# Kernel tuning notes

Measured on AMD Instinct MI355X. Metric: run time of the kernel, lower is better.

Reference implementation:

```python
import jax, jax.numpy as jnp
import numpy as np

N, DIN, HID, DOUT = 8192, 256, 256, 128   # nodes, gcn dims
B, L = 64, 64                              # ragged batch, max seq len
LH, C = 128, 4                             # lstm hidden, n_classes


def setup_inputs() -> dict:
    key = jax.random.key(0)
    ks = jax.random.split(key, 12)
    s = lambda k, shape, fan: jax.random.normal(k, shape, jnp.float32) / np.float32(np.sqrt(fan))
    A = jax.random.normal(ks[0], (N, N), jnp.float32) / np.float32(np.sqrt(N))
    X = jax.random.normal(ks[1], (N, DIN), jnp.float32)
    token_ids = jax.random.randint(ks[2], (B, L), 0, N, dtype=jnp.int32)
    lengths = jax.random.randint(ks[3], (B,), 1, L + 1, dtype=jnp.int32)
    return {
        'A': A, 'X': X, 'token_ids': token_ids, 'lengths': lengths,
        'W1': s(ks[4], (DIN, HID), DIN), 'b1': jnp.zeros((HID,), jnp.float32),
        'W2': s(ks[5], (HID, DOUT), HID), 'b2': jnp.zeros((DOUT,), jnp.float32),
        'Wih_f': s(ks[6], (4 * LH, DOUT), DOUT), 'Whh_f': s(ks[7], (4 * LH, LH), LH),
        'b_f': jnp.zeros((4 * LH,), jnp.float32),
        'Wih_b': s(ks[8], (4 * LH, DOUT), DOUT), 'Whh_b': s(ks[9], (4 * LH, LH), LH),
        'b_b': jnp.zeros((4 * LH,), jnp.float32),
        'Wfc': s(ks[10], (C, 2 * LH), 2 * LH), 'bfc': jnp.zeros((C,), jnp.float32),
    }


def _lstm_final(xp, mask, Whh):
    """xp: [L,B,4H] precomputed input gates, mask: [L,B]. Returns final valid h [B,H]."""
    Bsz = xp.shape[1]
    h0 = jnp.zeros((Bsz, Whh.shape[1]), xp.dtype)

    def step(carry, inp):
        h, c = carry
        xg, m = inp
        gates = xg + h @ Whh.T
        i, f, g, o = jnp.split(gates, 4, axis=-1)   # torch gate order i,f,g,o
        c_new = jax.nn.sigmoid(f) * c + jax.nn.sigmoid(i) * jnp.tanh(g)
        h_new = jax.nn.sigmoid(o) * jnp.tanh(c_new)
        m = m[:, None]
        return (jnp.where(m, h_new, h), jnp.where(m, c_new, c)), None

    (h, _), _ = jax.lax.scan(step, (h0, h0), (xp, mask))
    return h


def reference(A, X, token_ids, lengths, W1, b1, W2, b2,
              Wih_f, Whh_f, b_f, Wih_b, Whh_b, b_b, Wfc, bfc):
    # 2-layer GCN (num_layer=2 -> no middle layers / no relu); dropout in eval mode
    H1 = A @ (X @ W1) + b1                 # [N, HID]
    Hn = A @ (H1 @ W2) + b2                # [N, DOUT]
    seqs = Hn[token_ids]                   # ragged gather -> [B, L, DOUT]
    mask = (jnp.arange(L)[None, :] < lengths[:, None]).T            # [L, B]
    xp_f = jnp.einsum('bld,gd->lbg', seqs, Wih_f) + b_f             # [L, B, 4H]
    xp_b = jnp.einsum('bld,gd->lbg', seqs[:, ::-1], Wih_b) + b_b
    # backward dir: reversing a right-padded seq puts padding first; mask keeps
    # state frozen until the valid region, so final h == backward-final hidden.
    h_f = _lstm_final(xp_f, mask, Whh_f)
    h_b = _lstm_final(xp_b, mask[::-1], Whh_b)
    return jnp.concatenate([h_f, h_b], axis=-1) @ Wfc.T + bfc       # [B, C]
```

## Files before the change

kernel.cpp:

```cpp
#include <hip/hip_runtime.h>
#include <hip/hip_bf16.h>


typedef float f32x4 __attribute__((ext_vector_type(4)));
typedef __bf16 bf16x8 __attribute__((ext_vector_type(8)));
typedef unsigned short u16;
typedef unsigned int u32;

__device__ __forceinline__ u16 bf_hi_rn(float x, float& rem) {
    u32 u = __builtin_bit_cast(u32, x);
    u32 r = u + 0x7FFFu + ((u >> 16) & 1u);
    u16 h = (u16)(r >> 16);
    float hf = __builtin_bit_cast(float, (u32)h << 16);
    rem = x - hf;
    return h;
}
__device__ __forceinline__ u16 bf_trunc(float x) {
    return (u16)(__builtin_bit_cast(u32, x) >> 16);
}
__device__ __forceinline__ void pack8(const float* v, uint4& H, uint4& L) {
    u32 h[4], l[4];
#pragma unroll
    for (int q = 0; q < 4; q++) {
        float r0, r1;
        u32 h0 = bf_hi_rn(v[2 * q], r0);
        u32 h1 = bf_hi_rn(v[2 * q + 1], r1);
        h[q] = h0 | (h1 << 16);
        l[q] = (u32)bf_trunc(r0) | ((u32)bf_trunc(r1) << 16);
    }
    H = make_uint4(h[0], h[1], h[2], h[3]);
    L = make_uint4(l[0], l[1], l[2], l[3]);
}

__device__ __forceinline__ void glds16(const u16* g, u16* l) {
    __builtin_amdgcn_global_load_lds(
        (const __attribute__((address_space(1))) void*)g,
        (__attribute__((address_space(3))) void*)l, 16, 0, 0);
}

template<int TRANS>
__global__ void wsplit_k(const float* __restrict__ W, u16* __restrict__ hi,
                         u16* __restrict__ lo, int K, int N) {
    int gid = blockIdx.x * 256 + threadIdx.x;
    int total = (K >> 5) * N * 4;
    if (gid >= total) return;
    int g = gid & 3, n = (gid >> 2) % N, kc = gid / (4 * N);
    float v[8];
#pragma unroll
    for (int e = 0; e < 8; e++) {
        int k = kc * 32 + g * 8 + e;
        v[e] = TRANS ? W[(size_t)k * N + n] : W[(size_t)n * K + k];
    }
    uint4 H, L;
    pack8(v, H, L);
    int p = g ^ ((n >> 1) & 3);
    size_t off = ((size_t)kc * N + n) * 32 + p * 8;
    *(uint4*)(hi + off) = H;
    *(uint4*)(lo + off) = L;
}

template<int GMODE, int NPART, int BIASA, int SPLITOUT, int BIASC, int DUAL>
__global__ __launch_bounds__(512, 1) void gemm2_k(
    const float* __restrict__ A, int ldA, int Mtot,
    const u16* __restrict__ Bhi, const u16* __restrict__ Blo,
    const u16* __restrict__ Bhi2, const u16* __restrict__ Blo2, int Nfull,
    float* __restrict__ C, int ldC, long partStride,
    u16* __restrict__ Chi, u16* __restrict__ Clo, int Nout,
    const float* __restrict__ biasA,
    const float* __restrict__ biasC, const float* __restrict__ biasC2,
    const int* __restrict__ tok, int kchunk, int Mhalf)
{
    constexpr int BM = 256, BN = 128;
    const int t = threadIdx.x;
    const int lane = t & 63, wv = t >> 6;
    const int fm = lane & 15, fq = lane >> 4;
    const int wm0 = (wv >> 1) * 64, wn0 = (wv & 1) * 64;
    const int m0 = blockIdx.x * BM;
    const int n0 = blockIdx.z * BN;
    const int kbeg = blockIdx.y * kchunk;

    __shared__ alignas(16) u16 sAhi[2][BM * 32];
    __shared__ alignas(16) u16 sAlo[2][BM * 32];
    __shared__ alignas(16) u16 sBhi[2][BN * 32];
    __shared__ alignas(16) u16 sBlo[2][BN * 32];
    __shared__ int sRow[BM];

    if (t < BM) {
        int r;
        if (GMODE == 0) r = m0 + t;
        else if (GMODE == 1) r = tok[m0 + t];
        else {
            int trip = m0 + t;
            int rem = trip & (Mhalf - 1);
            int l = rem >> 6, b = rem & 63;
            r = (trip < Mhalf) ? (b * 64 + l) : (b * 64 + (63 - l));
        }
        sRow[t] = r;
    }
    __syncthreads();

    const bool second = DUAL && (m0 >= Mhalf);
    const u16* __restrict__ bhp = second ? Bhi2 : Bhi;
    const u16* __restrict__ blp = second ? Blo2 : Blo;

    const int r = t >> 1, half = t & 1, co = half * 16;
    const int sw = (r >> 1) & 3;
    const int p0 = (2 * half) ^ sw, p1 = (2 * half + 1) ^ sw;
    const float* Abase = A + (size_t)sRow[r] * ldA + co;
    const size_t pstep = (size_t)Mtot * ldA;

    const size_t bstep = (size_t)Nfull * 32;
    const u16* gbh = bhp + ((size_t)(kbeg >> 5) * Nfull + n0) * 32 + t * 8;
    const u16* gbl = blp + ((size_t)(kbeg >> 5) * Nfull + n0) * 32 + t * 8;
    u16* ldsBh0 = &sBhi[0][wv * 512];
    u16* ldsBl0 = &sBlo[0][wv * 512];
    u16* ldsBh1 = &sBhi[1][wv * 512];
    u16* ldsBl1 = &sBlo[1][wv * 512];

    f32x4 acc[4][4];
#pragma unroll
    for (int i = 0; i < 4; i++)
#pragma unroll
        for (int j = 0; j < 4; j++) acc[i][j] = (f32x4){0.f, 0.f, 0.f, 0.f};

    float av[16];
    auto loadA = [&](int kk) {
#pragma unroll
        for (int c = 0; c < 16; c += 4) {
            float4 s = *(const float4*)(Abase + kk + c);
            av[c] = s.x; av[c + 1] = s.y; av[c + 2] = s.z; av[c + 3] = s.w;
        }
#pragma unroll
        for (int p = 1; p < NPART; p++) {
#pragma unroll
            for (int c = 0; c < 16; c += 4) {
                float4 s = *(const float4*)(Abase + (size_t)p * pstep + kk + c);
                av[c] += s.x; av[c + 1] += s.y; av[c + 2] += s.z; av[c + 3] += s.w;
            }
        }
        if (BIASA) {
#pragma unroll
            for (int c = 0; c < 16; c += 4) {
                float4 s = *(const float4*)(biasA + kk + co + c);
                av[c] += s.x; av[c + 1] += s.y; av[c + 2] += s.z; av[c + 3] += s.w;
            }
        }
    };
    auto storeA = [&](int nb) {
        uint4 H0, L0, H1, L1;
        pack8(av, H0, L0);
        pack8(av + 8, H1, L1);
        int base = r * 32;
        *(uint4*)&sAhi[nb][base + p0 * 8] = H0;
        *(uint4*)&sAlo[nb][base + p0 * 8] = L0;
        *(uint4*)&sAhi[nb][base + p1 * 8] = H1;
        *(uint4*)&sAlo[nb][base + p1 * 8] = L1;
    };
    const int pf8 = (fq ^ ((fm >> 1) & 3)) * 8;
    auto compute = [&](int cur) {
        bf16x8 bh4[4], bl4[4];
#pragma unroll
        for (int j = 0; j < 4; j++) {
            int off = (wn0 + 16 * j + fm) * 32 + pf8;
            bh4[j] = *(const bf16x8*)&sBhi[cur][off];
            bl4[j] = *(const bf16x8*)&sBlo[cur][off];
        }
#pragma unroll
        for (int i = 0; i < 4; i++) {
            int off = (wm0 + 16 * i + fm) * 32 + pf8;
            bf16x8 ah = *(const bf16x8*)&sAhi[cur][off];
            bf16x8 al = *(const bf16x8*)&sAlo[cur][off];
#pragma unroll
            for (int j = 0; j < 4; j++) {
                acc[i][j] = __builtin_amdgcn_mfma_f32_16x16x32_bf16(ah, bh4[j], acc[i][j], 0, 0, 0);
                acc[i][j] = __builtin_amdgcn_mfma_f32_16x16x32_bf16(ah, bl4[j], acc[i][j], 0, 0, 0);
                acc[i][j] = __builtin_amdgcn_mfma_f32_16x16x32_bf16(al, bh4[j], acc[i][j], 0, 0, 0);
            }
        }
    };

    const int iters = kchunk >> 5;
    glds16(gbh, ldsBh0);
    glds16(gbl, ldsBl0);
    loadA(kbeg);
    storeA(0);
    __syncthreads();

#pragma unroll 1
    for (int k = 0; k < iters; k++) {
        const int cur = k & 1, nb = cur ^ 1;
        const bool pf = (k + 1 < iters);
        if (pf) {
            glds16(gbh + (size_t)(k + 1) * bstep, nb ? ldsBh1 : ldsBh0);
            glds16(gbl + (size_t)(k + 1) * bstep, nb ? ldsBl1 : ldsBl0);
            loadA(kbeg + (k + 1) * 32);
        }
        compute(cur);
        if (pf) storeA(nb);
        __syncthreads();
    }

    if (!SPLITOUT) {
        float* Cp = C + (size_t)blockIdx.y * partStride;
        const float* bc = second ? biasC2 : biasC;
#pragma unroll
        for (int i = 0; i < 4; i++)
#pragma unroll
            for (int j = 0; j < 4; j++)
#pragma unroll
                for (int rr = 0; rr < 4; rr++) {
                    int row = m0 + wm0 + 16 * i + fq * 4 + rr;
                    int col = n0 + wn0 + 16 * j + fm;
                    float v = acc[i][j][rr];
                    if (BIASC) v += bc[col];
                    Cp[(size_t)row * ldC + col] = v;
                }
    } else {
        float* scr = (float*)&sAhi[0][0];
        const int kc0 = m0 >> 5;
        const int n = t & (BN - 1), gs = t >> 7;
        const int ngl = n0 + n;
        const int pp = gs ^ ((ngl >> 1) & 3);
#pragma unroll 1
        for (int g8 = 0; g8 < BM / 32; g8++) {
            if ((wv >> 1) == (g8 >> 1)) {
                int ib = (g8 & 1) * 2;
#pragma unroll
                for (int i2 = 0; i2 < 2; i2++)
#pragma unroll
                    for (int j = 0; j < 4; j++)
#pragma unroll
                        for (int rr = 0; rr < 4; rr++)
                            scr[(i2 * 16 + fq * 4 + rr) * BN + wn0 + 16 * j + fm] =
                                acc[ib + i2][j][rr];
            }
            __syncthreads();
            float v[8];
#pragma unroll
            for (int e = 0; e < 8; e++) v[e] = scr[(gs * 8 + e) * BN + n];
            uint4 H, L;
            pack8(v, H, L);
            size_t off = ((size_t)(kc0 + g8) * Nout + ngl) * 32 + pp * 8;
            *(uint4*)(Chi + off) = H;
            *(uint4*)(Clo + off) = L;
            __syncthreads();
        }
    }
}

__device__ __forceinline__ float rl(float v, int l) {
    return __builtin_bit_cast(float, __builtin_amdgcn_readlane(__builtin_bit_cast(int, v), l));
}
__device__ __forceinline__ float fsigmoid(float x) { return 1.f / (1.f + __expf(-x)); }
__device__ __forceinline__ float ftanh(float x) {
    float e = __expf(2.f * x);
    return 1.f - 2.f / (e + 1.f);
}

__global__ __launch_bounds__(512, 2) void lstm_k(
    const float* __restrict__ xp,
    const float* __restrict__ Whh_f, const float* __restrict__ Whh_b,
    const int* __restrict__ lengths,
    float* __restrict__ hfin)
{
    const int bid = blockIdx.x;
    const int dir = bid >> 6;
    const int b = bid & 63;
    const int t = threadIdx.x;
    const int lane = t & 63, wv = t >> 6;
    const int gtype = wv >> 1;
    const float* Whh = dir ? Whh_b : Whh_f;
    const int len = lengths[b];

    float wr[128];
#pragma unroll
    for (int i = 0; i < 128; i += 4) {
        float4 v = *(const float4*)(Whh + t * 128 + i);
        wr[i] = v.x; wr[i + 1] = v.y; wr[i + 2] = v.z; wr[i + 3] = v.w;
    }

    __shared__ float gact[2][512];
    float h0 = 0.f, h1 = 0.f, c0 = 0.f, c1 = 0.f;
    const float* xpp = xp + ((size_t)dir * 4096 + b) * 512 + t;

    for (int l = 0; l < 64; l++) {
        float xg = xpp[(size_t)l * 32768];
        float a0 = xg, a1 = 0.f, a2 = 0.f, a3 = 0.f;
#pragma unroll
        for (int j = 0; j < 64; j += 2) {
            a0 = fmaf(wr[j], rl(h0, j), a0);
            a1 = fmaf(wr[j + 1], rl(h0, j + 1), a1);
        }
#pragma unroll
        for (int j = 0; j < 64; j += 2) {
            a2 = fmaf(wr[64 + j], rl(h1, j), a2);
            a3 = fmaf(wr[64 + j + 1], rl(h1, j + 1), a3);
        }
        float acc = (a0 + a1) + (a2 + a3);
        float act = (gtype == 2) ? ftanh(acc) : fsigmoid(acc);
        gact[l & 1][t] = act;
        __syncthreads();
        float iv0 = gact[l & 1][lane],       iv1 = gact[l & 1][64 + lane];
        float fv0 = gact[l & 1][128 + lane], fv1 = gact[l & 1][192 + lane];
        float gv0 = gact[l & 1][256 + lane], gv1 = gact[l & 1][320 + lane];
        float ov0 = gact[l & 1][384 + lane], ov1 = gact[l & 1][448 + lane];
        float cn0 = fv0 * c0 + iv0 * gv0;
        float cn1 = fv1 * c1 + iv1 * gv1;
        float hn0 = ov0 * ftanh(cn0);
        float hn1 = ov1 * ftanh(cn1);
        bool upd = ((dir == 0) ? l : (63 - l)) < len;
        if (upd) { c0 = cn0; c1 = cn1; h0 = hn0; h1 = hn1; }
    }
    if (wv == 0) {
        hfin[((size_t)dir * 64 + b) * 128 + lane] = h0;
        hfin[((size_t)dir * 64 + b) * 128 + 64 + lane] = h1;
    }
}

__global__ void fc_k(const float* __restrict__ hf, const float* __restrict__ Wfc,
                     const float* __restrict__ bfc, float* __restrict__ out) {
    int t = threadIdx.x;
    int b = t >> 2, c = t & 3;
    float s = bfc[c];
#pragma unroll 4
    for (int j = 0; j < 128; j++) s = fmaf(hf[b * 128 + j], Wfc[c * 256 + j], s);
#pragma unroll 4
    for (int j = 0; j < 128; j++) s = fmaf(hf[(64 + b) * 128 + j], Wfc[c * 256 + 128 + j], s);
    out[b * 4 + c] = s;
}

extern "C" void kernel_launch(void* const* d_in, const int* in_sizes, int n_in,
                              void* d_out, int out_size, void* d_ws, size_t ws_size,
                              hipStream_t stream) {
    const float* A     = (const float*)d_in[0];
    const float* X     = (const float*)d_in[1];
    const int*   tok   = (const int*)d_in[2];
    const int*   lens  = (const int*)d_in[3];
    const float* W1    = (const float*)d_in[4];
    const float* b1    = (const float*)d_in[5];
    const float* W2    = (const float*)d_in[6];
    const float* b2    = (const float*)d_in[7];
    const float* Wih_f = (const float*)d_in[8];
    const float* Whh_f = (const float*)d_in[9];
    const float* b_f   = (const float*)d_in[10];
    const float* Wih_b = (const float*)d_in[11];
    const float* Whh_b = (const float*)d_in[12];
    const float* b_b   = (const float*)d_in[13];
    const float* Wfc   = (const float*)d_in[14];
    const float* bfc   = (const float*)d_in[15];
    float* out = (float*)d_out;
    char* ws = (char*)d_ws;

    float* H1p  = (float*)(ws + 0);
    float* xp   = (float*)(ws + 0);
    u16*   B1hi = (u16*)(ws + 33554432);
    u16*   B1lo = (u16*)(ws + 37748736);
    u16*   B2hi = (u16*)(ws + 41943040);
    u16*   B2lo = (u16*)(ws + 44040192);
    float* sqP  = (float*)(ws + 46137344);
    float* hfin = (float*)(ws + 79691776);
    u16*   W1h  = (u16*)(ws + 79757312);
    u16*   W1l  = (u16*)(ws + 79888384);
    u16*   W2h  = (u16*)(ws + 80019456);
    u16*   W2l  = (u16*)(ws + 80084992);
    u16*   Wfh  = (u16*)(ws + 80150528);
    u16*   Wfl  = (u16*)(ws + 80281600);
    u16*   Wbh  = (u16*)(ws + 80412672);
    u16*   Wbl  = (u16*)(ws + 80543744);

    wsplit_k<1><<<32, 256, 0, stream>>>(W1, W1h, W1l, 256, 256);
    wsplit_k<1><<<16, 256, 0, stream>>>(W2, W2h, W2l, 256, 128);
    wsplit_k<0><<<32, 256, 0, stream>>>(Wih_f, Wfh, Wfl, 128, 512);
    wsplit_k<0><<<32, 256, 0, stream>>>(Wih_b, Wbh, Wbl, 128, 512);

    gemm2_k<0, 1, 0, 1, 0, 0><<<dim3(32, 1, 2), 512, 0, stream>>>(
        X, 256, 8192, W1h, W1l, nullptr, nullptr, 256,
        nullptr, 0, 0, B1hi, B1lo, 256,
        nullptr, nullptr, nullptr, nullptr, 256, 4096);
    gemm2_k<0, 1, 0, 0, 0, 0><<<dim3(32, 4, 2), 512, 0, stream>>>(
        A, 8192, 8192, B1hi, B1lo, nullptr, nullptr, 256,
        H1p, 256, (long)8192 * 256, nullptr, nullptr, 0,
        nullptr, nullptr, nullptr, nullptr, 2048, 4096);
    gemm2_k<0, 4, 1, 1, 0, 0><<<dim3(32, 1, 1), 512, 0, stream>>>(
        H1p, 256, 8192, W2h, W2l, nullptr, nullptr, 128,
        nullptr, 0, 0, B2hi, B2lo, 128,
        b1, nullptr, nullptr, nullptr, 256, 4096);
    gemm2_k<1, 1, 0, 0, 0, 0><<<dim3(16, 16, 1), 512, 0, stream>>>(
        A, 8192, 8192, B2hi, B2lo, nullptr, nullptr, 128,
        sqP, 128, (long)4096 * 128, nullptr, nullptr, 0,
        nullptr, nullptr, nullptr, tok, 512, 4096);
    gemm2_k<2, 16, 1, 0, 1, 1><<<dim3(32, 1, 4), 512, 0, stream>>>(
        sqP, 128, 4096, Wfh, Wfl, Wbh, Wbl, 512,
        xp, 512, 0, nullptr, nullptr, 0,
        b2, b_f, b_b, nullptr, 128, 4096);
    lstm_k<<<128, 512, 0, stream>>>(xp, Whh_f, Whh_b, lens, hfin);
    fc_k<<<1, 256, 0, stream>>>(hfin, Wfc, bfc, out);
}
```

Before: 817.2 us.

## Single-buffer A tile, raise occupancy, templatize BM, and deepen split-K

The GEMM kernel drops double buffering of the A tile in shared memory and raises launch bounds from 1 to 4 blocks per CU. The aim is to hide latency through more resident waves rather than software pipelining. It also makes BM a template parameter (BM=128 for the LSTM input projection, doubling its grid) and doubles the split-K factor on the first A GEMM from 4 to 8 partitions. The hi/lo bf16 split now truncates instead of rounding to nearest, and the workspace layout is rearranged. A global loads now sit behind an extra barrier, so they no longer overlap compute, and the extra split-K partials add reduction traffic in the next GEMM.

```diff
diff --git a/kernel.cpp b/kernel.cpp
--- a/kernel.cpp
+++ b/kernel.cpp
@@ -27,6 +27,21 @@
         u32 h1 = bf_hi_rn(v[2 * q + 1], r1);
         h[q] = h0 | (h1 << 16);
         l[q] = (u32)bf_trunc(r0) | ((u32)bf_trunc(r1) << 16);
+    }
+    H = make_uint4(h[0], h[1], h[2], h[3]);
+    L = make_uint4(l[0], l[1], l[2], l[3]);
+}
+__device__ __forceinline__ void pack8t(const float* v, uint4& H, uint4& L) {
+    u32 h[4], l[4];
+#pragma unroll
+    for (int q = 0; q < 4; q++) {
+        u32 u0 = __builtin_bit_cast(u32, v[2 * q]);
+        u32 u1 = __builtin_bit_cast(u32, v[2 * q + 1]);
+        h[q] = (u0 >> 16) | (u1 & 0xFFFF0000u);
+        float r0 = v[2 * q] - __builtin_bit_cast(float, u0 & 0xFFFF0000u);
+        float r1 = v[2 * q + 1] - __builtin_bit_cast(float, u1 & 0xFFFF0000u);
+        l[q] = (__builtin_bit_cast(u32, r0) >> 16) |
+               (__builtin_bit_cast(u32, r1) & 0xFFFF0000u);
     }
     H = make_uint4(h[0], h[1], h[2], h[3]);
     L = make_uint4(l[0], l[1], l[2], l[3]);
@@ -59,8 +74,8 @@
     *(uint4*)(lo + off) = L;
 }
 
-template<int GMODE, int NPART, int BIASA, int SPLITOUT, int BIASC, int DUAL>
-__global__ __launch_bounds__(512, 1) void gemm2_k(
+template<int BM, int GMODE, int NPART, int BIASA, int SPLITOUT, int BIASC, int DUAL>
+__global__ __launch_bounds__(512, 4) void gemm3_k(
     const float* __restrict__ A, int ldA, int Mtot,
     const u16* __restrict__ Bhi, const u16* __restrict__ Blo,
     const u16* __restrict__ Bhi2, const u16* __restrict__ Blo2, int Nfull,
@@ -70,17 +85,26 @@
     const float* __restrict__ biasC, const float* __restrict__ biasC2,
     const int* __restrict__ tok, int kchunk, int Mhalf)
 {
-    constexpr int BM = 256, BN = 128;
+    constexpr int BN = 128;
+    constexpr int WROWS = BM / 64;
+    constexpr int WCOLS = 8 / WROWS;
+    constexpr int WTN = BN / WCOLS;
+    constexpr int NT = WTN / 16;
+    constexpr int AF = BM / 16;
+    constexpr int TPR = 512 / BM;
+    constexpr int NG = AF / 8;
+
     const int t = threadIdx.x;
     const int lane = t & 63, wv = t >> 6;
     const int fm = lane & 15, fq = lane >> 4;
-    const int wm0 = (wv >> 1) * 64, wn0 = (wv & 1) * 64;
+    const int wm0 = (wv / WCOLS) * 64;
+    const int wn0 = (wv % WCOLS) * WTN;
     const int m0 = blockIdx.x * BM;
     const int n0 = blockIdx.z * BN;
     const int kbeg = blockIdx.y * kchunk;
 
-    __shared__ alignas(16) u16 sAhi[2][BM * 32];
-    __shared__ alignas(16) u16 sAlo[2][BM * 32];
+    __shared__ alignas(16) u16 sAhi[BM * 32];
+    __shared__ alignas(16) u16 sAlo[BM * 32];
     __shared__ alignas(16) u16 sBhi[2][BN * 32];
     __shared__ alignas(16) u16 sBlo[2][BN * 32];
     __shared__ int sRow[BM];
@@ -103,64 +127,59 @@
     const u16* __restrict__ bhp = second ? Bhi2 : Bhi;
     const u16* __restrict__ blp = second ? Blo2 : Blo;
 
-    const int r = t >> 1, half = t & 1, co = half * 16;
+    const int r = t / TPR, q = t % TPR, co = q * AF;
     const int sw = (r >> 1) & 3;
-    const int p0 = (2 * half) ^ sw, p1 = (2 * half + 1) ^ sw;
     const float* Abase = A + (size_t)sRow[r] * ldA + co;
     const size_t pstep = (size_t)Mtot * ldA;
 
     const size_t bstep = (size_t)Nfull * 32;
     const u16* gbh = bhp + ((size_t)(kbeg >> 5) * Nfull + n0) * 32 + t * 8;
     const u16* gbl = blp + ((size_t)(kbeg >> 5) * Nfull + n0) * 32 + t * 8;
-    u16* ldsBh0 = &sBhi[0][wv * 512];
-    u16* ldsBl0 = &sBlo[0][wv * 512];
-    u16* ldsBh1 = &sBhi[1][wv * 512];
-    u16* ldsBl1 = &sBlo[1][wv * 512];
-
-    f32x4 acc[4][4];
+
+    f32x4 acc[4][NT];
 #pragma unroll
     for (int i = 0; i < 4; i++)
 #pragma unroll
-        for (int j = 0; j < 4; j++) acc[i][j] = (f32x4){0.f, 0.f, 0.f, 0.f};
-
-    float av[16];
+        for (int j = 0; j < NT; j++) acc[i][j] = (f32x4){0.f, 0.f, 0.f, 0.f};
+
+    float av[AF];
     auto loadA = [&](int kk) {
 #pragma unroll
-        for (int c = 0; c < 16; c += 4) {
+        for (int c = 0; c < AF; c += 4) {
             float4 s = *(const float4*)(Abase + kk + c);
             av[c] = s.x; av[c + 1] = s.y; av[c + 2] = s.z; av[c + 3] = s.w;
         }
 #pragma unroll
         for (int p = 1; p < NPART; p++) {
 #pragma unroll
-            for (int c = 0; c < 16; c += 4) {
+            for (int c = 0; c < AF; c += 4) {
                 float4 s = *(const float4*)(Abase + (size_t)p * pstep + kk + c);
                 av[c] += s.x; av[c + 1] += s.y; av[c + 2] += s.z; av[c + 3] += s.w;
             }
         }
         if (BIASA) {
 #pragma unroll
-            for (int c = 0; c < 16; c += 4) {
+            for (int c = 0; c < AF; c += 4) {
                 float4 s = *(const float4*)(biasA + kk + co + c);
                 av[c] += s.x; av[c + 1] += s.y; av[c + 2] += s.z; av[c + 3] += s.w;
             }
         }
     };
-    auto storeA = [&](int nb) {
-        uint4 H0, L0, H1, L1;
-        pack8(av, H0, L0);
-        pack8(av + 8, H1, L1);
-        int base = r * 32;
-        *(uint4*)&sAhi[nb][base + p0 * 8] = H0;
-        *(uint4*)&sAlo[nb][base + p0 * 8] = L0;
-        *(uint4*)&sAhi[nb][base + p1 * 8] = H1;
-        *(uint4*)&sAlo[nb][base + p1 * 8] = L1;
+    auto storeA = [&]() {
+#pragma unroll
+        for (int g = 0; g < NG; g++) {
+            uint4 H, L;
+            pack8t(av + 8 * g, H, L);
+            int p = ((co >> 3) + g) ^ sw;
+            *(uint4*)&sAhi[r * 32 + p * 8] = H;
+            *(uint4*)&sAlo[r * 32 + p * 8] = L;
+        }
     };
     const int pf8 = (fq ^ ((fm >> 1) & 3)) * 8;
     auto compute = [&](int cur) {
-        bf16x8 bh4[4], bl4[4];
-#pragma unroll
-        for (int j = 0; j < 4; j++) {
+        bf16x8 bh4[NT], bl4[NT];
+#pragma unroll
+        for (int j = 0; j < NT; j++) {
             int off = (wn0 + 16 * j + fm) * 32 + pf8;
             bh4[j] = *(const bf16x8*)&sBhi[cur][off];
             bl4[j] = *(const bf16x8*)&sBlo[cur][off];
@@ -168,10 +187,10 @@
 #pragma unroll
         for (int i = 0; i < 4; i++) {
             int off = (wm0 + 16 * i + fm) * 32 + pf8;
-            bf16x8 ah = *(const bf16x8*)&sAhi[cur][off];
-            bf16x8 al = *(const bf16x8*)&sAlo[cur][off];
-#pragma unroll
-            for (int j = 0; j < 4; j++) {
+            bf16x8 ah = *(const bf16x8*)&sAhi[off];
+            bf16x8 al = *(const bf16x8*)&sAlo[off];
+#pragma unroll
+            for (int j = 0; j < NT; j++) {
                 acc[i][j] = __builtin_amdgcn_mfma_f32_16x16x32_bf16(ah, bh4[j], acc[i][j], 0, 0, 0);
                 acc[i][j] = __builtin_amdgcn_mfma_f32_16x16x32_bf16(ah, bl4[j], acc[i][j], 0, 0, 0);
                 acc[i][j] = __builtin_amdgcn_mfma_f32_16x16x32_bf16(al, bh4[j], acc[i][j], 0, 0, 0);
@@ -180,23 +199,26 @@
     };
 
     const int iters = kchunk >> 5;
-    glds16(gbh, ldsBh0);
-    glds16(gbl, ldsBl0);
     loadA(kbeg);
-    storeA(0);
+    glds16(gbh, &sBhi[0][wv * 512]);
+    glds16(gbl, &sBlo[0][wv * 512]);
+    storeA();
     __syncthreads();
 
 #pragma unroll 1
     for (int k = 0; k < iters; k++) {
-        const int cur = k & 1, nb = cur ^ 1;
+        const int cur = k & 1;
         const bool pf = (k + 1 < iters);
         if (pf) {
-            glds16(gbh + (size_t)(k + 1) * bstep, nb ? ldsBh1 : ldsBh0);
-            glds16(gbl + (size_t)(k + 1) * bstep, nb ? ldsBl1 : ldsBl0);
+            glds16(gbh + (size_t)(k + 1) * bstep, &sBhi[cur ^ 1][wv * 512]);
+            glds16(gbl + (size_t)(k + 1) * bstep, &sBlo[cur ^ 1][wv * 512]);
+        }
+        compute(cur);
+        __syncthreads();
+        if (pf) {
             loadA(kbeg + (k + 1) * 32);
-        }
-        compute(cur);
-        if (pf) storeA(nb);
+            storeA();
+        }
         __syncthreads();
     }
 
@@ -206,7 +228,7 @@
 #pragma unroll
         for (int i = 0; i < 4; i++)
 #pragma unroll
-            for (int j = 0; j < 4; j++)
+            for (int j = 0; j < NT; j++)
 #pragma unroll
                 for (int rr = 0; rr < 4; rr++) {
                     int row = m0 + wm0 + 16 * i + fq * 4 + rr;
@@ -216,9 +238,9 @@
                     Cp[(size_t)row * ldC + col] = v;
                 }
     } else {
-        float* scr = (float*)&sAhi[0][0];
+        float* scr = (float*)&sAhi[0];
         const int kc0 = m0 >> 5;
-        const int n = t & (BN - 1), gs = t >> 7;
+        const int n = t & 127, gs = t >> 7;
         const int ngl = n0 + n;
         const int pp = gs ^ ((ngl >> 1) & 3);
 #pragma unroll 1
@@ -228,7 +250,7 @@
 #pragma unroll
                 for (int i2 = 0; i2 < 2; i2++)
 #pragma unroll
-                    for (int j = 0; j < 4; j++)
+                    for (int j = 0; j < NT; j++)
 #pragma unroll
                         for (int rr = 0; rr < 4; rr++)
                             scr[(i2 * 16 + fq * 4 + rr) * BN + wn0 + 16 * j + fm] =
@@ -352,12 +374,12 @@
     char* ws = (char*)d_ws;
 
     float* H1p  = (float*)(ws + 0);
-    float* xp   = (float*)(ws + 0);
-    u16*   B1hi = (u16*)(ws + 33554432);
-    u16*   B1lo = (u16*)(ws + 37748736);
-    u16*   B2hi = (u16*)(ws + 41943040);
-    u16*   B2lo = (u16*)(ws + 44040192);
-    float* sqP  = (float*)(ws + 46137344);
+    float* sqP  = (float*)(ws + 0);
+    float* xp   = (float*)(ws + 33554432);
+    u16*   B1hi = (u16*)(ws + 67108864);
+    u16*   B1lo = (u16*)(ws + 71303168);
+    u16*   B2hi = (u16*)(ws + 75497472);
+    u16*   B2lo = (u16*)(ws + 77594624);
     float* hfin = (float*)(ws + 79691776);
     u16*   W1h  = (u16*)(ws + 79757312);
     u16*   W1l  = (u16*)(ws + 79888384);
@@ -373,23 +395,23 @@
     wsplit_k<0><<<32, 256, 0, stream>>>(Wih_f, Wfh, Wfl, 128, 512);
     wsplit_k<0><<<32, 256, 0, stream>>>(Wih_b, Wbh, Wbl, 128, 512);
 
-    gemm2_k<0, 1, 0, 1, 0, 0><<<dim3(32, 1, 2), 512, 0, stream>>>(
+    gemm3_k<256, 0, 1, 0, 1, 0, 0><<<dim3(32, 1, 2), 512, 0, stream>>>(
         X, 256, 8192, W1h, W1l, nullptr, nullptr, 256,
         nullptr, 0, 0, B1hi, B1lo, 256,
         nullptr, nullptr, nullptr, nullptr, 256, 4096);
-    gemm2_k<0, 1, 0, 0, 0, 0><<<dim3(32, 4, 2), 512, 0, stream>>>(
+    gemm3_k<256, 0, 1, 0, 0, 0, 0><<<dim3(32, 8, 2), 512, 0, stream>>>(
         A, 8192, 8192, B1hi, B1lo, nullptr, nullptr, 256,
         H1p, 256, (long)8192 * 256, nullptr, nullptr, 0,
-        nullptr, nullptr, nullptr, nullptr, 2048, 4096);
-    gemm2_k<0, 4, 1, 1, 0, 0><<<dim3(32, 1, 1), 512, 0, stream>>>(
+        nullptr, nullptr, nullptr, nullptr, 1024, 4096);
+    gemm3_k<256, 0, 8, 1, 1, 0, 0><<<dim3(32, 1, 1), 512, 0, stream>>>(
         H1p, 256, 8192, W2h, W2l, nullptr, nullptr, 128,
         nullptr, 0, 0, B2hi, B2lo, 128,
         b1, nullptr, nullptr, nullptr, 256, 4096);
-    gemm2_k<1, 1, 0, 0, 0, 0><<<dim3(16, 16, 1), 512, 0, stream>>>(
+    gemm3_k<256, 1, 1, 0, 0, 0, 0><<<dim3(16, 16, 1), 512, 0, stream>>>(
         A, 8192, 8192, B2hi, B2lo, nullptr, nullptr, 128,
         sqP, 128, (long)4096 * 128, nullptr, nullptr, 0,
         nullptr, nullptr, nullptr, tok, 512, 4096);
-    gemm2_k<2, 16, 1, 0, 1, 1><<<dim3(32, 1, 4), 512, 0, stream>>>(
+    gemm3_k<128, 2, 16, 1, 0, 1, 1><<<dim3(64, 1, 4), 512, 0, stream>>>(
         sqP, 128, 4096, Wfh, Wfl, Wbh, Wbl, 512,
         xp, 512, 0, nullptr, nullptr, 0,
         b2, b_f, b_b, nullptr, 128, 4096);
```

New measurement: 867.2 us. +6.1%, slower.
